# Kernel tuning notes

Hardware: AMD Instinct MI355X
Metric: run time of the kernel (lower is better)

## Reference

```python
import jax, jax.numpy as jnp
import numpy as np

EMBED_DIM = 1024
NUM_HEADS = 16
HEAD_DIM = EMBED_DIM // NUM_HEADS
ROPE_BASE = 10000.0


def setup_inputs() -> dict:
    key = jax.random.key(0)
    k1, k2, k3, k4, k5 = jax.random.split(key, 5)
    b, t = 4, 2048
    s = 1.0 / np.sqrt(EMBED_DIM)
    return {
        "query": jax.random.normal(k1, (b, t, EMBED_DIM), jnp.float32),
        "in_proj_w": jax.random.normal(k2, (3 * EMBED_DIM, EMBED_DIM), jnp.float32) * s,
        "in_proj_b": jax.random.normal(k3, (3 * EMBED_DIM,), jnp.float32) * 0.02,
        "out_proj_w": jax.random.normal(k4, (EMBED_DIM, EMBED_DIM), jnp.float32) * s,
        "out_proj_b": jax.random.normal(k5, (EMBED_DIM,), jnp.float32) * 0.02,
    }


def _rope_cos_sin(t: int, dtype):
    inv_freq = 1.0 / (ROPE_BASE ** (jnp.arange(0, HEAD_DIM, 2, dtype=jnp.float32) / HEAD_DIM))
    freqs = jnp.arange(t, dtype=jnp.float32)[:, None] * inv_freq[None, :]  # [t, hd/2]
    return jnp.cos(freqs).astype(dtype), jnp.sin(freqs).astype(dtype)


def _apply_rotary(x, cos, sin):
    # x: [b, h, t, hd]; cos/sin: [t, hd/2]
    x1 = x[..., ::2]
    x2 = x[..., 1::2]
    c = cos[None, None, :, :]
    s = sin[None, None, :, :]
    rotated = jnp.stack((x1 * c - x2 * s, x1 * s + x2 * c), axis=-1)  # [b,h,t,hd/2,2]
    return rotated.reshape(x.shape)


def reference(query, in_proj_w, in_proj_b, out_proj_w, out_proj_b):
    b, t, d = query.shape
    qkv = query @ in_proj_w.T + in_proj_b  # [b, t, 3d]
    q, k, v = jnp.split(qkv, 3, axis=-1)
    def heads(x):
        return x.reshape(b, t, NUM_HEADS, HEAD_DIM).transpose(0, 2, 1, 3)  # [b,h,t,hd]
    q, k, v = heads(q), heads(k), heads(v)
    cos, sin = _rope_cos_sin(t, query.dtype)
    q = _apply_rotary(q, cos, sin)
    k = _apply_rotary(k, cos, sin)
    scale = 1.0 / np.sqrt(HEAD_DIM)
    scores = jnp.einsum('bhqd,bhkd->bhqk', q, k) * scale  # [b,h,t,t]
    probs = jax.nn.softmax(scores, axis=-1)
    attn = jnp.einsum('bhqk,bhkd->bhqd', probs, v)
    out = attn.transpose(0, 2, 1, 3).reshape(b, t, d)
    return out @ out_proj_w.T + out_proj_b
```

## Files before the change

### kernel.cpp

```cpp
#include <hip/hip_runtime.h>
#include <hip/hip_bf16.h>

#define EMBED 1024
#define NHEADS 16
#define HDIM 64
#define BATCH 4
#define SEQ 2048
#define BT (BATCH*SEQ)
#define NQKV (3*EMBED)


typedef _Float16 f16;
typedef __attribute__((ext_vector_type(8))) _Float16 half8;
typedef __attribute__((ext_vector_type(4))) _Float16 half4;
typedef __attribute__((ext_vector_type(4))) float f32x4;
typedef __attribute__((ext_vector_type(16))) float f32x16;
typedef __attribute__((ext_vector_type(4))) unsigned int u32x4;

__device__ __forceinline__ f32x4 mfma16f(half8 a, half8 b, f32x4 c) {
    return __builtin_amdgcn_mfma_f32_16x16x32_f16(a, b, c, 0, 0, 0);
}
__device__ __forceinline__ f32x16 mfma32(half8 a, half8 b, f32x16 c) {
    return __builtin_amdgcn_mfma_f32_32x32x16_f16(a, b, c, 0, 0, 0);
}
__device__ __forceinline__ f32x16 z16() {
    f32x16 z;
    #pragma unroll
    for (int i = 0; i < 16; i++) z[i] = 0.f;
    return z;
}
__device__ __forceinline__ unsigned int pk16(float a, float b) {
    auto h = __builtin_amdgcn_cvt_pkrtz(a, b);
    return __builtin_bit_cast(unsigned int, h);
}
__device__ __forceinline__ half8 mk8(unsigned int w0, unsigned int w1,
                                     unsigned int w2, unsigned int w3) {
    u32x4 v = (u32x4){w0, w1, w2, w3};
    return __builtin_bit_cast(half8, v);
}
__device__ __forceinline__ void pswap(unsigned int &a, unsigned int &b) {
    asm("v_permlane32_swap_b32 %0, %1" : "+v"(a), "+v"(b));
}

__device__ __forceinline__ half8 cvt8(float4 a, float4 b) {
    half8 r;
    r[0] = (f16)a.x; r[1] = (f16)a.y; r[2] = (f16)a.z; r[3] = (f16)a.w;
    r[4] = (f16)b.x; r[5] = (f16)b.y; r[6] = (f16)b.z; r[7] = (f16)b.w;
    return r;
}

__device__ __forceinline__ void gload16(const void* g, void* l) {
    __builtin_amdgcn_global_load_lds(
        (const __attribute__((address_space(1))) void*)g,
        (__attribute__((address_space(3))) void*)l, 16, 0, 0);
}

__global__ __launch_bounds__(256) void cvt_kernel(
    const float* __restrict__ X, const float* __restrict__ W1,
    const float* __restrict__ W2, f16* __restrict__ Xh,
    f16* __restrict__ W1h, f16* __restrict__ W2h, float2* __restrict__ CSt)
{
    const int u0 = blockIdx.x * 256 + threadIdx.x;
    #pragma unroll
    for (int i = 0; i < 3; i++) {
        const size_t uu = (size_t)u0 + (size_t)i * 524288;
        const float* src; f16* dst; size_t off;
        if (uu < 1048576)      { src = X;  dst = Xh;  off = uu * 8; }
        else if (uu < 1441792) { src = W1; dst = W1h; off = (uu - 1048576) * 8; }
        else                   { src = W2; dst = W2h; off = (uu - 1441792) * 8; }
        float4 a = *(const float4*)(src + off);
        float4 b = *(const float4*)(src + off + 4);
        *(half8*)(dst + off) = cvt8(a, b);
    }
    if (u0 < SEQ * 32) {
        const int t = u0 >> 5, fi = u0 & 31;
        const float ang = (float)t * exp2f(-0.41524103f * (float)fi);
        CSt[u0] = make_float2(cosf(ang), sinf(ang));
    }
}

__global__ __launch_bounds__(256) void qkv_rope_kernel(
    const f16* __restrict__ Xh, const f16* __restrict__ Wh,
    const float* __restrict__ bias, const float2* __restrict__ CSt,
    f16* __restrict__ Qg, f16* __restrict__ Kg, f16* __restrict__ Vtg)
{
    __shared__ __align__(16) char smem[65536];
    f16* A0 = (f16*)smem;
    f16* B0 = (f16*)(smem + 16384);
    f16* A1 = (f16*)(smem + 32768);
    f16* B1 = (f16*)(smem + 49152);
    f16 (*Ep)[136] = (f16(*)[136])smem;

    const int tid = threadIdx.x;

    const int L   = blockIdx.y * 24 + blockIdx.x;
    const int nw  = (L & 7) * 192 + (L >> 3);
    const int m0  = (nw / 24) * 128;
    const int n0  = (nw % 24) * 128;

    const int lane = tid & 63;
    const int wv = tid >> 6, wm = wv >> 1, wn = wv & 1;
    const int quad = lane >> 4, l15 = lane & 15;
    const int sw = (l15 & 7) << 4;

    const int srow  = tid >> 3;
    const int sslot = (tid & 7) ^ (srow & 7);
    const f16* asrc = Xh + (size_t)(m0 + srow) * EMBED + sslot * 8;
    const f16* bsrc = Wh + (size_t)(n0 + srow) * EMBED + sslot * 8;

    f32x4 acc[4][4];
    #pragma unroll
    for (int i = 0; i < 4; i++)
        #pragma unroll
        for (int j = 0; j < 4; j++) acc[i][j] = (f32x4){0.f,0.f,0.f,0.f};

    #pragma unroll
    for (int i = 0; i < 4; i++) {
        gload16(asrc + (size_t)i*32*EMBED, A0 + i*2048 + tid*8);
        gload16(bsrc + (size_t)i*32*EMBED, B0 + i*2048 + tid*8);
    }
    __syncthreads();

    for (int t = 0; t < 16; t++) {
        const f16* Ac = (t & 1) ? A1 : A0;
        const f16* Bc = (t & 1) ? B1 : B0;
        if (t < 15) {
            f16* An = (t & 1) ? A0 : A1;
            f16* Bn = (t & 1) ? B0 : B1;
            const int k0 = (t + 1) * 64;
            #pragma unroll
            for (int i = 0; i < 4; i++) {
                gload16(asrc + (size_t)i*32*EMBED + k0, An + i*2048 + tid*8);
                gload16(bsrc + (size_t)i*32*EMBED + k0, Bn + i*2048 + tid*8);
            }
        }

        half8 bf[4][2];
        #pragma unroll
        for (int nj = 0; nj < 4; nj++) {
            const int rb = wn*64 + nj*16 + l15;
            bf[nj][0] = *(const half8*)((const char*)Bc + rb*128 + ((quad*16) ^ sw));
            bf[nj][1] = *(const half8*)((const char*)Bc + rb*128 + ((64 + quad*16) ^ sw));
        }
        #pragma unroll
        for (int mi = 0; mi < 4; mi++) {
            const int ra = wm*64 + mi*16 + l15;
            half8 a0 = *(const half8*)((const char*)Ac + ra*128 + ((quad*16) ^ sw));
            half8 a1 = *(const half8*)((const char*)Ac + ra*128 + ((64 + quad*16) ^ sw));
            #pragma unroll
            for (int nj = 0; nj < 4; nj++) {
                acc[mi][nj] = mfma16f(a0, bf[nj][0], acc[mi][nj]);
                acc[mi][nj] = mfma16f(a1, bf[nj][1], acc[mi][nj]);
            }
        }
        __syncthreads();
    }

    const int sect = n0 >> 10;
    const int h0   = (n0 & 1023) >> 6;
    const int bb   = m0 >> 11, t0 = m0 & 2047;

    #pragma unroll
    for (int mi = 0; mi < 4; mi++) {
        #pragma unroll
        for (int nj = 0; nj < 4; nj++) {
            const int ncol = wn*64 + nj*16 + l15;
            const int hd = ncol & 63;
            const float bz = bias[n0 + ncol];
            #pragma unroll
            for (int r = 0; r < 4; r++) {
                const int tl = wm*64 + mi*16 + quad*4 + r;
                float v = acc[mi][nj][r] + bz;
                if (sect < 2) {
                    float partner = __shfl_xor(v, 1, 64);
                    float2 cs2 = CSt[(t0 + tl)*32 + (hd >> 1)];
                    float o = (hd & 1) ? fmaf(partner, cs2.y, v * cs2.x)
                                       : fmaf(v, cs2.x, -(partner * cs2.y));
                    Ep[tl][ncol] = (f16)o;
                } else {
                    Ep[ncol][tl] = (f16)v;
                }
            }
        }
    }
    __syncthreads();

    const int orow = tid >> 1;
    const int oc   = (tid & 1) * 64;
    f16* dst;
    if (sect == 2) {
        const int h = h0 + (orow >> 6), d = orow & 63;
        dst = Vtg + ((size_t)((bb*NHEADS + h) * HDIM + d)) * SEQ + t0 + oc;
    } else {
        const int h = h0 + (tid & 1);
        f16* base = (sect == 0) ? Qg : Kg;
        dst = base + ((size_t)((bb*NHEADS + h) * SEQ + t0 + orow)) * HDIM;
    }
    #pragma unroll
    for (int c8 = 0; c8 < 8; c8++)
        *(half8*)(dst + c8*8) = *(const half8*)&Ep[orow][oc + c8*8];
}

__global__ __launch_bounds__(128, 2) void attn_kernel(
    const f16* __restrict__ Qg, const f16* __restrict__ Kg,
    const f16* __restrict__ Vtg, f16* __restrict__ Ow)
{
    __shared__ __align__(16) f16 KV[2][2][64*64];

    const int tid  = threadIdx.x;
    const int lane = tid & 63, wq = tid >> 6;
    const int hi   = lane >> 5, col = lane & 31;

    const int lin = blockIdx.y * 16 + blockIdx.x;
    const int bh  = (lin & 7) + ((lin >> 7) << 3);
    const int qb  = (lin >> 3) & 15;
    const int q0  = qb * 128;

    const f16* Kb = Kg  + (size_t)bh * SEQ * HDIM;
    const f16* Vb = Vtg + (size_t)bh * HDIM * SEQ;

    const int r8   = tid >> 3;
    const int slot = tid & 7;

    #pragma unroll
    for (int g = 0; g < 4; g++) {
        const int row = g*16 + r8;
        const int sc  = (slot ^ (row & 7)) * 8;
        gload16(Kb + (size_t)row * HDIM + sc, &KV[0][0][0] + g*1024 + tid*8);
        gload16(Vb + (size_t)row * SEQ  + sc, &KV[0][1][0] + g*1024 + tid*8);
    }

    half8 qf[2][4];
    #pragma unroll
    for (int nb = 0; nb < 2; nb++) {
        const f16* qsrc = Qg + (size_t)bh * SEQ * HDIM
                        + (size_t)(q0 + wq*64 + nb*32 + col) * HDIM + hi*8;
        #pragma unroll
        for (int kc = 0; kc < 4; kc++)
            qf[nb][kc] = *(const half8*)(qsrc + kc*16);
    }

    f32x16 oacc[2][2];
    oacc[0][0] = z16(); oacc[0][1] = z16();
    oacc[1][0] = z16(); oacc[1][1] = z16();
    float lsum[2] = {0.f, 0.f};

    __syncthreads();

    for (int it = 0; it < 32; it++) {
        const f16* kl = &KV[it & 1][0][0];
        const f16* vl = &KV[it & 1][1][0];

        if (it < 31) {
            f16* kd = &KV[(it + 1) & 1][0][0];
            f16* vd = &KV[(it + 1) & 1][1][0];
            const int j0n = (it + 1) * 64;
            #pragma unroll
            for (int g = 0; g < 4; g++) {
                const int row = g*16 + r8;
                const int sc  = (slot ^ (row & 7)) * 8;
                gload16(Kb + (size_t)(j0n + row) * HDIM + sc, kd + g*1024 + tid*8);
                gload16(Vb + (size_t)row * SEQ + j0n + sc,    vd + g*1024 + tid*8);
            }
        }

        half8 kf[2][4];
        #pragma unroll
        for (int jb = 0; jb < 2; jb++) {
            const int row = jb*32 + col;
            const char* base = (const char*)kl + row*128;
            const int sz = (row & 7) << 4;
            #pragma unroll
            for (int kc = 0; kc < 4; kc++)
                kf[jb][kc] = *(const half8*)(base + ((kc*32 + hi*16) ^ sz));
        }

        unsigned int pw[2][4][4];
        #pragma unroll
        for (int nb = 0; nb < 2; nb++) {
            f32x16 s0 = z16(), s1 = z16();
            __builtin_amdgcn_s_setprio(1);
            #pragma unroll
            for (int kc = 0; kc < 4; kc++) s0 = mfma32(kf[0][kc], qf[nb][kc], s0);
            #pragma unroll
            for (int kc = 0; kc < 4; kc++) s1 = mfma32(kf[1][kc], qf[nb][kc], s1);
            __builtin_amdgcn_s_setprio(0);

            float e0[16], e1[16];
            #pragma unroll
            for (int r = 0; r < 16; r++) {
                e0[r] = __expf(fmaf(s0[r], 0.125f, -4.0f));
                e1[r] = __expf(fmaf(s1[r], 0.125f, -4.0f));
            }
            float t00 = (e0[0]+e0[1]) + (e0[2]+e0[3]);
            float t01 = (e0[4]+e0[5]) + (e0[6]+e0[7]);
            float t02 = (e0[8]+e0[9]) + (e0[10]+e0[11]);
            float t03 = (e0[12]+e0[13]) + (e0[14]+e0[15]);
            float t10 = (e1[0]+e1[1]) + (e1[2]+e1[3]);
            float t11 = (e1[4]+e1[5]) + (e1[6]+e1[7]);
            float t12 = (e1[8]+e1[9]) + (e1[10]+e1[11]);
            float t13 = (e1[12]+e1[13]) + (e1[14]+e1[15]);
            lsum[nb] += ((t00+t01)+(t02+t03)) + ((t10+t11)+(t12+t13));

            unsigned int a, b;
            a = pk16(e0[0],  e0[1]);  b = pk16(e0[4],  e0[5]);
            pswap(a, b); pw[nb][0][0] = a; pw[nb][0][2] = b;
            a = pk16(e0[2],  e0[3]);  b = pk16(e0[6],  e0[7]);
            pswap(a, b); pw[nb][0][1] = a; pw[nb][0][3] = b;
            a = pk16(e0[8],  e0[9]);  b = pk16(e0[12], e0[13]);
            pswap(a, b); pw[nb][1][0] = a; pw[nb][1][2] = b;
            a = pk16(e0[10], e0[11]); b = pk16(e0[14], e0[15]);
            pswap(a, b); pw[nb][1][1] = a; pw[nb][1][3] = b;

            a = pk16(e1[0],  e1[1]);  b = pk16(e1[4],  e1[5]);
            pswap(a, b); pw[nb][2][0] = a; pw[nb][2][2] = b;
            a = pk16(e1[2],  e1[3]);  b = pk16(e1[6],  e1[7]);
            pswap(a, b); pw[nb][2][1] = a; pw[nb][2][3] = b;
            a = pk16(e1[8],  e1[9]);  b = pk16(e1[12], e1[13]);
            pswap(a, b); pw[nb][3][0] = a; pw[nb][3][2] = b;
            a = pk16(e1[10], e1[11]); b = pk16(e1[14], e1[15]);
            pswap(a, b); pw[nb][3][1] = a; pw[nb][3][3] = b;
        }

        __builtin_amdgcn_s_setprio(1);
        #pragma unroll
        for (int kc2 = 0; kc2 < 4; kc2++) {
            half8 pb0 = mk8(pw[0][kc2][0], pw[0][kc2][1], pw[0][kc2][2], pw[0][kc2][3]);
            half8 pb1 = mk8(pw[1][kc2][0], pw[1][kc2][1], pw[1][kc2][2], pw[1][kc2][3]);
            #pragma unroll
            for (int db = 0; db < 2; db++) {
                const int row = db*32 + col;
                const int sz = (row & 7) << 4;
                half8 vf = *(const half8*)((const char*)vl + row*128
                                           + ((kc2*32 + hi*16) ^ sz));
                oacc[db][0] = mfma32(vf, pb0, oacc[db][0]);
                oacc[db][1] = mfma32(vf, pb1, oacc[db][1]);
            }
        }
        __builtin_amdgcn_s_setprio(0);

        __syncthreads();
    }

    float invl[2];
    invl[0] = 1.0f / (lsum[0] + __shfl_xor(lsum[0], 32, 64));
    invl[1] = 1.0f / (lsum[1] + __shfl_xor(lsum[1], 32, 64));

    const int bb = bh >> 4, h = bh & 15;
    #pragma unroll
    for (int nb = 0; nb < 2; nb++) {
        const int t = q0 + wq*64 + nb*32 + col;
        f16* od = Ow + (size_t)(bb*SEQ + t) * EMBED + h*HDIM + hi*4;
        #pragma unroll
        for (int db = 0; db < 2; db++) {
            #pragma unroll
            for (int rg = 0; rg < 4; rg++) {
                half4 o;
                o[0] = (f16)(oacc[db][nb][rg*4+0] * invl[nb]);
                o[1] = (f16)(oacc[db][nb][rg*4+1] * invl[nb]);
                o[2] = (f16)(oacc[db][nb][rg*4+2] * invl[nb]);
                o[3] = (f16)(oacc[db][nb][rg*4+3] * invl[nb]);
                *(half4*)(od + db*32 + rg*8) = o;
            }
        }
    }
}

__global__ __launch_bounds__(256) void outproj_kernel(
    const f16* __restrict__ Aw, const f16* __restrict__ Wh,
    const float* __restrict__ bias, float* __restrict__ Out)
{
    __shared__ __align__(16) char smem[65536];
    f16* A0 = (f16*)smem;
    f16* B0 = (f16*)(smem + 16384);
    f16* A1 = (f16*)(smem + 32768);
    f16* B1 = (f16*)(smem + 49152);

    const int tid = threadIdx.x;

    const int L   = blockIdx.y * 8 + blockIdx.x;
    const int nw  = (L & 7) * 64 + (L >> 3);
    const int m0  = (nw / 8) * 128;
    const int n0  = (nw % 8) * 128;

    const int lane = tid & 63;
    const int wv = tid >> 6, wm = wv >> 1, wn = wv & 1;
    const int quad = lane >> 4, l15 = lane & 15;
    const int sw = (l15 & 7) << 4;

    const int srow  = tid >> 3;
    const int sslot = (tid & 7) ^ (srow & 7);
    const f16* asrc = Aw + (size_t)(m0 + srow) * EMBED + sslot * 8;
    const f16* bsrc = Wh + (size_t)(n0 + srow) * EMBED + sslot * 8;

    f32x4 acc[4][4];
    #pragma unroll
    for (int i = 0; i < 4; i++)
        #pragma unroll
        for (int j = 0; j < 4; j++) acc[i][j] = (f32x4){0.f,0.f,0.f,0.f};

    #pragma unroll
    for (int i = 0; i < 4; i++) {
        gload16(asrc + (size_t)i*32*EMBED, A0 + i*2048 + tid*8);
        gload16(bsrc + (size_t)i*32*EMBED, B0 + i*2048 + tid*8);
    }
    __syncthreads();

    for (int t = 0; t < 16; t++) {
        const f16* Ac = (t & 1) ? A1 : A0;
        const f16* Bc = (t & 1) ? B1 : B0;
        if (t < 15) {
            f16* An = (t & 1) ? A0 : A1;
            f16* Bn = (t & 1) ? B0 : B1;
            const int k0 = (t + 1) * 64;
            #pragma unroll
            for (int i = 0; i < 4; i++) {
                gload16(asrc + (size_t)i*32*EMBED + k0, An + i*2048 + tid*8);
                gload16(bsrc + (size_t)i*32*EMBED + k0, Bn + i*2048 + tid*8);
            }
        }

        half8 bf[4][2];
        #pragma unroll
        for (int nj = 0; nj < 4; nj++) {
            const int rb = wn*64 + nj*16 + l15;
            bf[nj][0] = *(const half8*)((const char*)Bc + rb*128 + ((quad*16) ^ sw));
            bf[nj][1] = *(const half8*)((const char*)Bc + rb*128 + ((64 + quad*16) ^ sw));
        }
        #pragma unroll
        for (int mi = 0; mi < 4; mi++) {
            const int ra = wm*64 + mi*16 + l15;
            half8 a0 = *(const half8*)((const char*)Ac + ra*128 + ((quad*16) ^ sw));
            half8 a1 = *(const half8*)((const char*)Ac + ra*128 + ((64 + quad*16) ^ sw));
            #pragma unroll
            for (int nj = 0; nj < 4; nj++) {
                acc[mi][nj] = mfma16f(a0, bf[nj][0], acc[mi][nj]);
                acc[mi][nj] = mfma16f(a1, bf[nj][1], acc[mi][nj]);
            }
        }
        __syncthreads();
    }

    #pragma unroll
    for (int mi = 0; mi < 4; mi++) {
        #pragma unroll
        for (int nj = 0; nj < 4; nj++) {
            const int n = n0 + wn*64 + nj*16 + l15;
            const float bz = bias[n];
            #pragma unroll
            for (int r = 0; r < 4; r++) {
                const int m = m0 + wm*64 + mi*16 + quad*4 + r;
                Out[(size_t)m * EMBED + n] = acc[mi][nj][r] + bz;
            }
        }
    }
}

extern "C" void kernel_launch(void* const* d_in, const int* in_sizes, int n_in,
                              void* d_out, int out_size, void* d_ws, size_t ws_size,
                              hipStream_t stream)
{
    const float* query = (const float*)d_in[0];
    const float* in_w  = (const float*)d_in[1];
    const float* in_b  = (const float*)d_in[2];
    const float* out_w = (const float*)d_in[3];
    const float* out_b = (const float*)d_in[4];
    float* out = (float*)d_out;

    const size_t NT = (size_t)BATCH * NHEADS * SEQ * HDIM;
    char* ws = (char*)d_ws;
    f16* Qg  = (f16*)ws;
    f16* Kg  = (f16*)(ws + 2*NT);
    f16* Vtg = (f16*)(ws + 4*NT);
    f16* Aw  = (f16*)(ws + 6*NT);
    f16* Xh  = (f16*)(ws + 6*NT);
    f16* W1h = (f16*)(ws + 8*NT);
    f16* W2h = (f16*)(ws + 8*NT + 6291456);
    float2* CSt = (float2*)(ws + 8*NT + 6291456 + 2097152);

    cvt_kernel<<<2048, 256, 0, stream>>>(query, in_w, out_w, Xh, W1h, W2h, CSt);
    dim3 g1(NQKV / 128, BT / 128);
    qkv_rope_kernel<<<g1, 256, 0, stream>>>(Xh, W1h, in_b, CSt, Qg, Kg, Vtg);
    dim3 g2(SEQ / 128, BATCH * NHEADS);
    attn_kernel<<<g2, 128, 0, stream>>>(Qg, Kg, Vtg, Aw);
    dim3 g3(EMBED / 128, BT / 128);
    outproj_kernel<<<g3, 256, 0, stream>>>(Aw, W2h, out_b, out);
}
```

Measured before the change: 332.4 us.

## Use 512-thread blocks with 8 waves per 128x128 tile in both GEMMs

```diff
diff --git a/kernel.cpp b/kernel.cpp
--- a/kernel.cpp
+++ b/kernel.cpp
@@ -79,7 +79,7 @@
     }
 }
 
-__global__ __launch_bounds__(256) void qkv_rope_kernel(
+__global__ __launch_bounds__(512, 4) void qkv_rope_kernel(
     const f16* __restrict__ Xh, const f16* __restrict__ Wh,
     const float* __restrict__ bias, const float2* __restrict__ CSt,
     f16* __restrict__ Qg, f16* __restrict__ Kg, f16* __restrict__ Vtg)
@@ -92,33 +92,28 @@
     f16 (*Ep)[136] = (f16(*)[136])smem;
 
     const int tid = threadIdx.x;
-
-    const int L   = blockIdx.y * 24 + blockIdx.x;
-    const int nw  = (L & 7) * 192 + (L >> 3);
-    const int m0  = (nw / 24) * 128;
-    const int n0  = (nw % 24) * 128;
-
+    const int m0 = blockIdx.y * 128, n0 = blockIdx.x * 128;
     const int lane = tid & 63;
-    const int wv = tid >> 6, wm = wv >> 1, wn = wv & 1;
+    const int wv = tid >> 6;
+    const int wm = wv >> 2, wn = wv & 3;
     const int quad = lane >> 4, l15 = lane & 15;
     const int sw = (l15 & 7) << 4;
 
-    const int srow  = tid >> 3;
-    const int sslot = (tid & 7) ^ (srow & 7);
-    const f16* asrc = Xh + (size_t)(m0 + srow) * EMBED + sslot * 8;
-    const f16* bsrc = Wh + (size_t)(n0 + srow) * EMBED + sslot * 8;
-
-    f32x4 acc[4][4];
+    const int rlo   = tid >> 3;
+    const int sslot = (tid & 7) ^ (rlo & 7);
+    const f16* asrc = Xh + (size_t)(m0 + rlo) * EMBED + sslot * 8;
+    const f16* bsrc = Wh + (size_t)(n0 + rlo) * EMBED + sslot * 8;
+
+    f32x4 acc[4][2];
     #pragma unroll
     for (int i = 0; i < 4; i++)
         #pragma unroll
-        for (int j = 0; j < 4; j++) acc[i][j] = (f32x4){0.f,0.f,0.f,0.f};
-
-    #pragma unroll
-    for (int i = 0; i < 4; i++) {
-        gload16(asrc + (size_t)i*32*EMBED, A0 + i*2048 + tid*8);
-        gload16(bsrc + (size_t)i*32*EMBED, B0 + i*2048 + tid*8);
-    }
+        for (int j = 0; j < 2; j++) acc[i][j] = (f32x4){0.f,0.f,0.f,0.f};
+
+    gload16(asrc,                      A0 + tid*8);
+    gload16(asrc + (size_t)64*EMBED,   A0 + 4096 + tid*8);
+    gload16(bsrc,                      B0 + tid*8);
+    gload16(bsrc + (size_t)64*EMBED,   B0 + 4096 + tid*8);
     __syncthreads();
 
     for (int t = 0; t < 16; t++) {
@@ -128,17 +123,16 @@
             f16* An = (t & 1) ? A0 : A1;
             f16* Bn = (t & 1) ? B0 : B1;
             const int k0 = (t + 1) * 64;
-            #pragma unroll
-            for (int i = 0; i < 4; i++) {
-                gload16(asrc + (size_t)i*32*EMBED + k0, An + i*2048 + tid*8);
-                gload16(bsrc + (size_t)i*32*EMBED + k0, Bn + i*2048 + tid*8);
-            }
-        }
-
-        half8 bf[4][2];
-        #pragma unroll
-        for (int nj = 0; nj < 4; nj++) {
-            const int rb = wn*64 + nj*16 + l15;
+            gload16(asrc + k0,                    An + tid*8);
+            gload16(asrc + (size_t)64*EMBED + k0, An + 4096 + tid*8);
+            gload16(bsrc + k0,                    Bn + tid*8);
+            gload16(bsrc + (size_t)64*EMBED + k0, Bn + 4096 + tid*8);
+        }
+
+        half8 bf[2][2];
+        #pragma unroll
+        for (int nj = 0; nj < 2; nj++) {
+            const int rb = wn*32 + nj*16 + l15;
             bf[nj][0] = *(const half8*)((const char*)Bc + rb*128 + ((quad*16) ^ sw));
             bf[nj][1] = *(const half8*)((const char*)Bc + rb*128 + ((64 + quad*16) ^ sw));
         }
@@ -148,7 +142,7 @@
             half8 a0 = *(const half8*)((const char*)Ac + ra*128 + ((quad*16) ^ sw));
             half8 a1 = *(const half8*)((const char*)Ac + ra*128 + ((64 + quad*16) ^ sw));
             #pragma unroll
-            for (int nj = 0; nj < 4; nj++) {
+            for (int nj = 0; nj < 2; nj++) {
                 acc[mi][nj] = mfma16f(a0, bf[nj][0], acc[mi][nj]);
                 acc[mi][nj] = mfma16f(a1, bf[nj][1], acc[mi][nj]);
             }
@@ -163,8 +157,8 @@
     #pragma unroll
     for (int mi = 0; mi < 4; mi++) {
         #pragma unroll
-        for (int nj = 0; nj < 4; nj++) {
-            const int ncol = wn*64 + nj*16 + l15;
+        for (int nj = 0; nj < 2; nj++) {
+            const int ncol = wn*32 + nj*16 + l15;
             const int hd = ncol & 63;
             const float bz = bias[n0 + ncol];
             #pragma unroll
@@ -185,19 +179,19 @@
     }
     __syncthreads();
 
-    const int orow = tid >> 1;
-    const int oc   = (tid & 1) * 64;
+    const int orow = tid >> 2;
+    const int oc   = (tid & 3) * 32;
     f16* dst;
     if (sect == 2) {
         const int h = h0 + (orow >> 6), d = orow & 63;
         dst = Vtg + ((size_t)((bb*NHEADS + h) * HDIM + d)) * SEQ + t0 + oc;
     } else {
-        const int h = h0 + (tid & 1);
+        const int h = h0 + (oc >> 6);
         f16* base = (sect == 0) ? Qg : Kg;
-        dst = base + ((size_t)((bb*NHEADS + h) * SEQ + t0 + orow)) * HDIM;
-    }
-    #pragma unroll
-    for (int c8 = 0; c8 < 8; c8++)
+        dst = base + ((size_t)((bb*NHEADS + h) * SEQ + t0 + orow)) * HDIM + (oc & 63);
+    }
+    #pragma unroll
+    for (int c8 = 0; c8 < 4; c8++)
         *(half8*)(dst + c8*8) = *(const half8*)&Ep[orow][oc + c8*8];
 }
 
@@ -366,7 +360,7 @@
     }
 }
 
-__global__ __launch_bounds__(256) void outproj_kernel(
+__global__ __launch_bounds__(512, 4) void outproj_kernel(
     const f16* __restrict__ Aw, const f16* __restrict__ Wh,
     const float* __restrict__ bias, float* __restrict__ Out)
 {
@@ -377,33 +371,28 @@
     f16* B1 = (f16*)(smem + 49152);
 
     const int tid = threadIdx.x;
-
-    const int L   = blockIdx.y * 8 + blockIdx.x;
-    const int nw  = (L & 7) * 64 + (L >> 3);
-    const int m0  = (nw / 8) * 128;
-    const int n0  = (nw % 8) * 128;
-
+    const int m0 = blockIdx.y * 128, n0 = blockIdx.x * 128;
     const int lane = tid & 63;
-    const int wv = tid >> 6, wm = wv >> 1, wn = wv & 1;
+    const int wv = tid >> 6;
+    const int wm = wv >> 2, wn = wv & 3;
     const int quad = lane >> 4, l15 = lane & 15;
     const int sw = (l15 & 7) << 4;
 
-    const int srow  = tid >> 3;
-    const int sslot = (tid & 7) ^ (srow & 7);
-    const f16* asrc = Aw + (size_t)(m0 + srow) * EMBED + sslot * 8;
-    const f16* bsrc = Wh + (size_t)(n0 + srow) * EMBED + sslot * 8;
-
-    f32x4 acc[4][4];
+    const int rlo   = tid >> 3;
+    const int sslot = (tid & 7) ^ (rlo & 7);
+    const f16* asrc = Aw + (size_t)(m0 + rlo) * EMBED + sslot * 8;
+    const f16* bsrc = Wh + (size_t)(n0 + rlo) * EMBED + sslot * 8;
+
+    f32x4 acc[4][2];
     #pragma unroll
     for (int i = 0; i < 4; i++)
         #pragma unroll
-        for (int j = 0; j < 4; j++) acc[i][j] = (f32x4){0.f,0.f,0.f,0.f};
-
-    #pragma unroll
-    for (int i = 0; i < 4; i++) {
-        gload16(asrc + (size_t)i*32*EMBED, A0 + i*2048 + tid*8);
-        gload16(bsrc + (size_t)i*32*EMBED, B0 + i*2048 + tid*8);
-    }
+        for (int j = 0; j < 2; j++) acc[i][j] = (f32x4){0.f,0.f,0.f,0.f};
+
+    gload16(asrc,                      A0 + tid*8);
+    gload16(asrc + (size_t)64*EMBED,   A0 + 4096 + tid*8);
+    gload16(bsrc,                      B0 + tid*8);
+    gload16(bsrc + (size_t)64*EMBED,   B0 + 4096 + tid*8);
     __syncthreads();
 
     for (int t = 0; t < 16; t++) {
@@ -413,17 +402,16 @@
             f16* An = (t & 1) ? A0 : A1;
             f16* Bn = (t & 1) ? B0 : B1;
             const int k0 = (t + 1) * 64;
-            #pragma unroll
-            for (int i = 0; i < 4; i++) {
-                gload16(asrc + (size_t)i*32*EMBED + k0, An + i*2048 + tid*8);
-                gload16(bsrc + (size_t)i*32*EMBED + k0, Bn + i*2048 + tid*8);
-            }
-        }
-
-        half8 bf[4][2];
-        #pragma unroll
-        for (int nj = 0; nj < 4; nj++) {
-            const int rb = wn*64 + nj*16 + l15;
+            gload16(asrc + k0,                    An + tid*8);
+            gload16(asrc + (size_t)64*EMBED + k0, An + 4096 + tid*8);
+            gload16(bsrc + k0,                    Bn + tid*8);
+            gload16(bsrc + (size_t)64*EMBED + k0, Bn + 4096 + tid*8);
+        }
+
+        half8 bf[2][2];
+        #pragma unroll
+        for (int nj = 0; nj < 2; nj++) {
+            const int rb = wn*32 + nj*16 + l15;
             bf[nj][0] = *(const half8*)((const char*)Bc + rb*128 + ((quad*16) ^ sw));
             bf[nj][1] = *(const half8*)((const char*)Bc + rb*128 + ((64 + quad*16) ^ sw));
         }
@@ -433,7 +421,7 @@
             half8 a0 = *(const half8*)((const char*)Ac + ra*128 + ((quad*16) ^ sw));
             half8 a1 = *(const half8*)((const char*)Ac + ra*128 + ((64 + quad*16) ^ sw));
             #pragma unroll
-            for (int nj = 0; nj < 4; nj++) {
+            for (int nj = 0; nj < 2; nj++) {
                 acc[mi][nj] = mfma16f(a0, bf[nj][0], acc[mi][nj]);
                 acc[mi][nj] = mfma16f(a1, bf[nj][1], acc[mi][nj]);
             }
@@ -444,8 +432,8 @@
     #pragma unroll
     for (int mi = 0; mi < 4; mi++) {
         #pragma unroll
-        for (int nj = 0; nj < 4; nj++) {
-            const int n = n0 + wn*64 + nj*16 + l15;
+        for (int nj = 0; nj < 2; nj++) {
+            const int n = n0 + wn*32 + nj*16 + l15;
             const float bz = bias[n];
             #pragma unroll
             for (int r = 0; r < 4; r++) {
@@ -480,9 +468,9 @@
 
     cvt_kernel<<<2048, 256, 0, stream>>>(query, in_w, out_w, Xh, W1h, W2h, CSt);
     dim3 g1(NQKV / 128, BT / 128);
-    qkv_rope_kernel<<<g1, 256, 0, stream>>>(Xh, W1h, in_b, CSt, Qg, Kg, Vtg);
+    qkv_rope_kernel<<<g1, 512, 0, stream>>>(Xh, W1h, in_b, CSt, Qg, Kg, Vtg);
     dim3 g2(SEQ / 128, BATCH * NHEADS);
     attn_kernel<<<g2, 128, 0, stream>>>(Qg, Kg, Vtg, Aw);
     dim3 g3(EMBED / 128, BT / 128);
-    outproj_kernel<<<g3, 256, 0, stream>>>(Aw, W2h, out_b, out);
-}
+    outproj_kernel<<<g3, 512, 0, stream>>>(Aw, W2h, out_b, out);
+}
```

Result: faster. 316.4 us (-4.8%).
